# Performance work log

Hardware: AMD Instinct MI355X
Metric: run time of the kernel (lower is better)

## Reference

```python
import jax, jax.numpy as jnp
import numpy as np

# Production-scale dims (see shape_source)
B, C, H, W = 4, 128, 64, 64
RADIUS = 0.2
TEMP = 0.1
PAD_VALUE = 0.0
P = int(H * RADIUS) * 2 + 1  # local window size kH = kW = 25


def setup_inputs() -> dict:
    key = jax.random.key(0)
    k1, k2 = jax.random.split(key)
    query = jax.random.normal(k1, (B, C, H, W), dtype=jnp.float32)
    keys = jax.random.normal(k2, (B, C, H, W), dtype=jnp.float32)
    return {"query": query, "keys": keys}


def _make_idx_map(h_dim, w_dim, p):
    # Equivalent of F.unfold(arange(H*W).view(H,W), kernel=(P,P), pad=P//2).clamp(min=0)
    # idx[h, w, p1, p2] = linear index of (h+p1-P//2, w+p2-P//2), 0 if out of bounds
    off = np.arange(p) - p // 2
    hh = np.arange(h_dim)[:, None, None, None] + off[None, None, :, None]  # (H,1,P,1)
    ww = np.arange(w_dim)[None, :, None, None] + off[None, None, None, :]  # (1,W,1,P)
    valid = (hh >= 0) & (hh < h_dim) & (ww >= 0) & (ww < w_dim)
    idx = np.where(valid, hh * w_dim + ww, 0)  # (H,W,P,P)
    return jnp.asarray(idx.reshape(h_dim * w_dim, p * p), dtype=jnp.int32)

_IDX_MAP = _make_idx_map(H, W, P)  # (H*W, P*P) int32 constant


def _local_correlation(query, keys, p):
    # spatial_correlation_sample(kernel=1, patch=P, stride=1, pad=0, dilation=1):
    # att[b,p1,p2,h,w] = sum_c query[b,c,h,w] * keys_zero_padded[b,c,h+p1-P//2,w+p2-P//2]
    pad = p // 2
    keys_pad = jnp.pad(keys, ((0, 0), (0, 0), (pad, pad), (pad, pad)))

    def corr_one(i):
        p1, p2 = i // p, i % p
        k = jax.lax.dynamic_slice(keys_pad, (0, 0, p1, p2), keys.shape)
        return jnp.einsum('bchw,bchw->bhw', query, k)

    att = jax.lax.map(corr_one, jnp.arange(p * p))  # (P*P, B, H, W); sequential keeps memory low
    return jnp.transpose(att, (1, 2, 3, 0))  # b h w (p1 p2)


def reference(query, keys):
    n_pix = H * W
    att = _local_correlation(query, keys, P) / TEMP  # (B,H,W,P*P)
    # knn(): pad_value==0, topk==0 -> mask exact zeros (out-of-window zero-padded corrs) to -10
    A = jnp.where(att == PAD_VALUE, jnp.float32(-10.0), att)
    A = jnp.exp(A.reshape(B, n_pix, P * P))  # b (h w) n
    # scatter_add into dense (B, H*W, H*W) affinity map
    q_idx = jnp.arange(n_pix)[:, None]  # (HW,1)
    out = jnp.zeros((B, n_pix, n_pix), dtype=A.dtype)
    out = out.at[:, q_idx, _IDX_MAP].add(A)
    # rearr 'b (h w) n -> b n h w'
    return out.reshape(B, H, W, n_pix).transpose(0, 3, 1, 2)
```

## Files before the change

### kernel.cpp

```cpp
#include <hip/hip_runtime.h>
#include <math.h>


#define BDIM 256
constexpr int Bn = 4, Cc = 128, Hh = 64, Ww = 64, HW = 4096;
constexpr int P = 25, Rr = 12, T = 8;

__device__ __forceinline__ int cntf(int x) {
    int c = P;
    if (x < Rr) c -= (Rr - x);
    if (x > (Hh - 1 - Rr)) c -= (x - (Hh - 1 - Rr));
    return c;
}

__global__ __launch_bounds__(BDIM) void localwalk_kernel(
    const float* __restrict__ query, const float* __restrict__ keys,
    float* __restrict__ out)
{
    const int jt = blockIdx.x;
    const int jh = blockIdx.y;
    const int b  = blockIdx.z;
    const int jw0 = jt * T;
    const int t = threadIdx.x;

    __shared__ float S[T * P * P];

    const float E10 = expf(-10.0f);
    const bool special = (jh == 0) && (jt == 0);

    const float* kb = keys + (size_t)b * Cc * HW + jh * Ww + jw0;
    for (int i = t; i < Cc * T; i += BDIM)
        S[i] = kb[(size_t)(i >> 3) * HW + (i & 7)];
    __syncthreads();

    const int wloc = t & 31, hs = t >> 5;
    const int w = jw0 - Rr + wloc;
    const int wa = min(max(w, 0), Ww - 1);
    const bool wvalid = (w >= 0) && (w < Ww);

    int ha[4]; bool hv[4];
    #pragma unroll
    for (int r = 0; r < 4; ++r) {
        int hloc = hs + 8 * r;
        int h = jh - Rr + hloc;
        hv[r] = (hloc < P) && (h >= 0) && (h < Hh);
        ha[r] = min(max(h, 0), Hh - 1);
    }

    float acc[4][T];
    #pragma unroll
    for (int r = 0; r < 4; ++r)
        #pragma unroll
        for (int jj = 0; jj < T; ++jj) acc[r][jj] = 0.f;

    const float* qb = query + (size_t)b * Cc * HW;
    int qoff[4];
    #pragma unroll
    for (int r = 0; r < 4; ++r) qoff[r] = ha[r] * Ww + wa;

    #pragma unroll 4
    for (int c = 0; c < Cc; ++c) {
        const float* qc = qb + (size_t)c * HW;
        float qv[4];
        #pragma unroll
        for (int r = 0; r < 4; ++r) qv[r] = qc[qoff[r]];
        float4 k0 = *(const float4*)&S[c * 8];
        float4 k1 = *(const float4*)&S[c * 8 + 4];
        float kk[T] = {k0.x, k0.y, k0.z, k0.w, k1.x, k1.y, k1.z, k1.w};
        #pragma unroll
        for (int jj = 0; jj < T; ++jj)
            #pragma unroll
            for (int r = 0; r < 4; ++r)
                acc[r][jj] = fmaf(qv[r], kk[jj], acc[r][jj]);
    }

    __syncthreads();

    #pragma unroll
    for (int jj = 0; jj < T; ++jj) {
        const int d = wloc - jj;
        const bool dv = (d >= 0) && (d < P) && wvalid;
        #pragma unroll
        for (int r = 0; r < 4; ++r) {
            if (!dv || !hv[r]) continue;
            float att = acc[r][jj] / 0.1f;
            if (att == 0.0f) att = -10.0f;
            att = fminf(att, 88.0f);
            S[(jj * P + (hs + 8 * r)) * P + d] = expf(att);
        }
    }
    __syncthreads();

    float4* orow4 = (float4*)(out + ((size_t)(b * HW + jh * Ww + jw0)) * HW);
    for (int k = 0; k < 32; ++k) {
        int fi = t + k * BDIM;
        int jj  = fi >> 10;
        int idx = fi & 1023;
        int h   = idx >> 4;
        int w4  = (idx & 15) * 4;
        int hl  = h - (jh - Rr);
        bool hin = (hl >= 0) && (hl < P);

        float4 v = make_float4(0.f, 0.f, 0.f, 0.f);
        if (special && jj == 0) {
            int ch = cntf(h);
            v.x = (float)(P * P - ch * cntf(w4 + 0)) * E10;
            v.y = (float)(P * P - ch * cntf(w4 + 1)) * E10;
            v.z = (float)(P * P - ch * cntf(w4 + 2)) * E10;
            v.w = (float)(P * P - ch * cntf(w4 + 3)) * E10;
        }
        if (hin) {
            int base = (jj * P + hl) * P;
            int off  = jw0 + jj - Rr;
            int we0  = w4 - off;
            if ((unsigned)(we0 + 0) < (unsigned)P) v.x += S[base + we0 + 0];
            if ((unsigned)(we0 + 1) < (unsigned)P) v.y += S[base + we0 + 1];
            if ((unsigned)(we0 + 2) < (unsigned)P) v.z += S[base + we0 + 2];
            if ((unsigned)(we0 + 3) < (unsigned)P) v.w += S[base + we0 + 3];
        }
        orow4[fi] = v;
    }
}

extern "C" void kernel_launch(void* const* d_in, const int* in_sizes, int n_in,
                              void* d_out, int out_size, void* d_ws, size_t ws_size,
                              hipStream_t stream) {
    const float* query = (const float*)d_in[0];
    const float* keys  = (const float*)d_in[1];
    float* out = (float*)d_out;
    dim3 grid(Ww / T, Hh, Bn);
    localwalk_kernel<<<grid, dim3(BDIM), 0, stream>>>(query, keys, out);
}
```

Measured before the change: 385.6 us.

## Compute local correlation with bf16 MFMA instead of scalar FMA loop

Measured after the change: 420.0 us. 8.9% more time.

```diff
diff --git a/kernel.cpp b/kernel.cpp
--- a/kernel.cpp
+++ b/kernel.cpp
@@ -6,11 +6,27 @@
 constexpr int Bn = 4, Cc = 128, Hh = 64, Ww = 64, HW = 4096;
 constexpr int P = 25, Rr = 12, T = 8;
 
+typedef __attribute__((ext_vector_type(8))) short short8;
+typedef __attribute__((ext_vector_type(4))) float f32x4;
+
 __device__ __forceinline__ int cntf(int x) {
     int c = P;
     if (x < Rr) c -= (Rr - x);
     if (x > (Hh - 1 - Rr)) c -= (x - (Hh - 1 - Rr));
     return c;
+}
+
+__device__ __forceinline__ unsigned pkbf(unsigned hi, unsigned lo) {
+    return __builtin_amdgcn_perm(hi, lo, 0x07060302);
+}
+
+__device__ __forceinline__ short8 mkfrag(const unsigned u[8]) {
+    union { unsigned w[4]; short8 s; } x;
+    x.w[0] = pkbf(u[1], u[0]);
+    x.w[1] = pkbf(u[3], u[2]);
+    x.w[2] = pkbf(u[5], u[4]);
+    x.w[3] = pkbf(u[7], u[6]);
+    return x.s;
 }
 
 __global__ __launch_bounds__(BDIM) void localwalk_kernel(
@@ -22,6 +38,7 @@
     const int b  = blockIdx.z;
     const int jw0 = jt * T;
     const int t = threadIdx.x;
+    const int lane = t & 63, wv = t >> 6;
 
     __shared__ float S[T * P * P];
 
@@ -33,60 +50,68 @@
         S[i] = kb[(size_t)(i >> 3) * HW + (i & 7)];
     __syncthreads();
 
-    const int wloc = t & 31, hs = t >> 5;
-    const int w = jw0 - Rr + wloc;
-    const int wa = min(max(w, 0), Ww - 1);
-    const bool wvalid = (w >= 0) && (w < Ww);
-
-    int ha[4]; bool hv[4];
+    const int kgrp = lane >> 4;
+    const int bcol = min(lane & 15, T - 1);
+    short8 Bfrag[4];
     #pragma unroll
-    for (int r = 0; r < 4; ++r) {
-        int hloc = hs + 8 * r;
-        int h = jh - Rr + hloc;
-        hv[r] = (hloc < P) && (h >= 0) && (h < Hh);
-        ha[r] = min(max(h, 0), Hh - 1);
+    for (int q = 0; q < 4; ++q) {
+        unsigned u[8];
+        #pragma unroll
+        for (int e = 0; e < 8; ++e)
+            u[e] = __float_as_uint(S[(q * 32 + kgrp * 8 + e) * T + bcol]);
+        Bfrag[q] = mkfrag(u);
     }
 
-    float acc[4][T];
+    const float* qb = query + (size_t)b * Cc * HW;
+    f32x4 acc[16];
     #pragma unroll
-    for (int r = 0; r < 4; ++r)
+    for (int m = 0; m < 16; ++m) acc[m] = (f32x4){0.f, 0.f, 0.f, 0.f};
+
+    const int arow = lane & 15;
+    #pragma unroll
+    for (int m = 0; m < 16; ++m) {
+        const int tm   = wv * 16 + m;
+        const int hl   = tm >> 1;
+        const int h    = jh - Rr + hl;
+        const int hA   = min(max(h, 0), Hh - 1);
+        const int wloc = (tm & 1) * 16 + arow;
+        const int w    = jw0 - Rr + wloc;
+        const int wA   = min(max(w, 0), Ww - 1);
+        const float* qp = qb + (size_t)(kgrp * 8) * HW + hA * Ww + wA;
         #pragma unroll
-        for (int jj = 0; jj < T; ++jj) acc[r][jj] = 0.f;
-
-    const float* qb = query + (size_t)b * Cc * HW;
-    int qoff[4];
-    #pragma unroll
-    for (int r = 0; r < 4; ++r) qoff[r] = ha[r] * Ww + wa;
-
-    #pragma unroll 4
-    for (int c = 0; c < Cc; ++c) {
-        const float* qc = qb + (size_t)c * HW;
-        float qv[4];
-        #pragma unroll
-        for (int r = 0; r < 4; ++r) qv[r] = qc[qoff[r]];
-        float4 k0 = *(const float4*)&S[c * 8];
-        float4 k1 = *(const float4*)&S[c * 8 + 4];
-        float kk[T] = {k0.x, k0.y, k0.z, k0.w, k1.x, k1.y, k1.z, k1.w};
-        #pragma unroll
-        for (int jj = 0; jj < T; ++jj)
+        for (int q = 0; q < 4; ++q) {
+            const float* pc = qp + (size_t)q * 32 * HW;
+            unsigned u[8];
             #pragma unroll
-            for (int r = 0; r < 4; ++r)
-                acc[r][jj] = fmaf(qv[r], kk[jj], acc[r][jj]);
+            for (int e = 0; e < 8; ++e)
+                u[e] = __float_as_uint(pc[e * HW]);
+            acc[m] = __builtin_amdgcn_mfma_f32_16x16x32_bf16(mkfrag(u), Bfrag[q], acc[m], 0, 0, 0);
+        }
     }
 
     __syncthreads();
 
-    #pragma unroll
-    for (int jj = 0; jj < T; ++jj) {
-        const int d = wloc - jj;
-        const bool dv = (d >= 0) && (d < P) && wvalid;
+    const int jj = lane & 15;
+    if (jj < T) {
         #pragma unroll
-        for (int r = 0; r < 4; ++r) {
-            if (!dv || !hv[r]) continue;
-            float att = acc[r][jj] / 0.1f;
-            if (att == 0.0f) att = -10.0f;
-            att = fminf(att, 88.0f);
-            S[(jj * P + (hs + 8 * r)) * P + d] = expf(att);
+        for (int m = 0; m < 16; ++m) {
+            const int tm  = wv * 16 + m;
+            const int hl  = tm >> 1;
+            const int h   = jh - Rr + hl;
+            const bool hok = (hl < P) && (h >= 0) && (h < Hh);
+            const int wb2 = (tm & 1) * 16 + (lane >> 4) * 4;
+            #pragma unroll
+            for (int r = 0; r < 4; ++r) {
+                const int wloc = wb2 + r;
+                const int w = jw0 - Rr + wloc;
+                const int d = wloc - jj;
+                if (hok && (unsigned)d < (unsigned)P && (unsigned)w < (unsigned)Ww) {
+                    float att = acc[m][r] / 0.1f;
+                    if (att == 0.0f) att = -10.0f;
+                    att = fminf(att, 88.0f);
+                    S[(jj * P + hl) * P + d] = expf(att);
+                }
+            }
         }
     }
     __syncthreads();
@@ -94,7 +119,7 @@
     float4* orow4 = (float4*)(out + ((size_t)(b * HW + jh * Ww + jw0)) * HW);
     for (int k = 0; k < 32; ++k) {
         int fi = t + k * BDIM;
-        int jj  = fi >> 10;
+        int jjd = fi >> 10;
         int idx = fi & 1023;
         int h   = idx >> 4;
         int w4  = (idx & 15) * 4;
@@ -102,7 +127,7 @@
         bool hin = (hl >= 0) && (hl < P);
 
         float4 v = make_float4(0.f, 0.f, 0.f, 0.f);
-        if (special && jj == 0) {
+        if (special && jjd == 0) {
             int ch = cntf(h);
             v.x = (float)(P * P - ch * cntf(w4 + 0)) * E10;
             v.y = (float)(P * P - ch * cntf(w4 + 1)) * E10;
@@ -110,8 +135,8 @@
             v.w = (float)(P * P - ch * cntf(w4 + 3)) * E10;
         }
         if (hin) {
-            int base = (jj * P + hl) * P;
-            int off  = jw0 + jj - Rr;
+            int base = (jjd * P + hl) * P;
+            int off  = jw0 + jjd - Rr;
             int we0  = w4 - off;
             if ((unsigned)(we0 + 0) < (unsigned)P) v.x += S[base + we0 + 0];
             if ((unsigned)(we0 + 1) < (unsigned)P) v.y += S[base + we0 + 1];
```
